# Performance work log

Hardware: AMD Instinct MI355X
Metric: run time of the kernel (lower is better)

Reference implementation:

```python
import jax, jax.numpy as jnp
import numpy as np

B, C, H = 16, 256, 32          # batch, in_channels(=out_channels), image_size
HEADS, HS = 8, 32              # heads = out_channels // head_size
D = HEADS * HS                 # head_dim = 256
N = H * H                      # tokens = 1024
EPS = 1e-5


def _rel_indices(h, w):
    # Faithful port of RelativeAttention2d.get_indices
    y = np.arange(h)
    x = np.arange(w)
    y1, x1, y2, x2 = np.meshgrid(y, x, y, x, indexing='ij')
    idx = (y1 - y2 + h - 1) * (2 * w - 1) + (x1 - x2 + w - 1)
    return jnp.asarray(idx.reshape(-1), dtype=jnp.int32)  # [N*N]


def setup_inputs() -> dict:
    key = jax.random.key(0)
    ks = jax.random.split(key, 10)
    s = 0.02
    return {
        'x': jax.random.normal(ks[0], (B, C, H, H), jnp.float32),
        'ln_g': jnp.ones((C,), jnp.float32),
        'ln_b': jnp.zeros((C,), jnp.float32),
        'wq': jax.random.normal(ks[1], (D, C), jnp.float32) * s,
        'bq': jnp.zeros((D,), jnp.float32),
        'wk': jax.random.normal(ks[2], (D, C), jnp.float32) * s,
        'bk': jnp.zeros((D,), jnp.float32),
        'wv': jax.random.normal(ks[3], (D, C), jnp.float32) * s,
        'bv': jnp.zeros((D,), jnp.float32),
        'wo': jax.random.normal(ks[4], (C, D), jnp.float32) * s,
        'bo': jnp.zeros((C,), jnp.float32),
        'rel_bias': jax.random.normal(ks[5], (HEADS, (2 * H - 1) * (2 * H - 1)), jnp.float32),
        'rel_idx': _rel_indices(H, H),
    }


def reference(x, ln_g, ln_b, wq, bq, wk, bk, wv, bv, wo, bo, rel_bias, rel_idx):
    b = x.shape[0]
    # norm(): LayerNorm over channel axis (dim 1 after the double transpose)
    mu = jnp.mean(x, axis=1, keepdims=True)
    var = jnp.mean((x - mu) ** 2, axis=1, keepdims=True)
    xn = (x - mu) / jnp.sqrt(var + EPS)
    xn = xn * ln_g[None, :, None, None] + ln_b[None, :, None, None]
    # reshape_for_linear: raw reshape [b, C, H, W] -> [b, N, C] (as in torch)
    xr = xn.reshape(b, N, C)
    # projections, then raw view(b, heads, head_size, -1) as in torch
    q = (xr @ wq.T + bq).reshape(b, HEADS, HS, N)
    k = (xr @ wk.T + bk).reshape(b, HEADS, HS, N)
    v = (xr @ wv.T + bv).reshape(b, HEADS, HS, N)
    # dots = k^T q / sqrt(head_dim)   [b, heads, N, N]
    dots = jnp.einsum('bhdn,bhdm->bhnm', k, q) / np.float32(np.sqrt(D))
    # gathered relative position bias  [heads, N, N]
    bias = rel_bias[:, rel_idx].reshape(HEADS, N, N)
    attn = jax.nn.softmax(dots + bias[None], axis=-2)  # non-standard softmax dim
    # out = v @ attn  [b, heads, head_size, N]
    out = jnp.einsum('bhdn,bhnm->bhdm', v, attn)
    out = out.reshape(b, H, H, D)  # raw view as in torch
    out = out @ wo.T + bo          # to_output linear (dropout is identity in eval)
    out = out.reshape(b, C, H, H)  # raw view back to [b, out_channels, H, W]
    return x + out
```

## Files before the change

kernel.cpp:

```cpp
#include <hip/hip_runtime.h>
#include <cstdint>

#define PERB 262144

typedef __attribute__((ext_vector_type(8))) short bf16x8;
typedef __attribute__((ext_vector_type(4))) float f32x4;
typedef unsigned short ushort_t;

__device__ __forceinline__ uint16_t f2bf(float f) {
    uint32_t u = __float_as_uint(f);
    u += 0x7fff + ((u >> 16) & 1);
    return (uint16_t)(u >> 16);
}

__global__ __launch_bounds__(256) void prep_kernel(
    const float* __restrict__ x, const float* __restrict__ gam,
    const float* __restrict__ bet, ushort_t* __restrict__ X,
    const float* __restrict__ wq, const float* __restrict__ wk,
    const float* __restrict__ wv, const float* __restrict__ wo,
    ushort_t* __restrict__ oq, ushort_t* __restrict__ ok,
    ushort_t* __restrict__ ov, ushort_t* __restrict__ oo)
{
    const int blk = blockIdx.x;
    const int tid = threadIdx.x;
    if (blk < 256) {
        const int which = blk >> 6;
        const int idx = ((blk & 63) * 256 + tid) * 4;
        const float* src = which == 0 ? wq : which == 1 ? wk : which == 2 ? wv : wo;
        ushort_t* dst    = which == 0 ? oq : which == 1 ? ok : which == 2 ? ov : oo;
        const float4 v = *(const float4*)&src[idx];
        uint2 p;
        p.x = (uint32_t)f2bf(v.x) | ((uint32_t)f2bf(v.y) << 16);
        p.y = (uint32_t)f2bf(v.z) | ((uint32_t)f2bf(v.w) << 16);
        *(uint2*)&dst[idx] = p;
        return;
    }
    const int lb  = blk - 256;
    const int b   = lb >> 5;
    const int sp0 = (lb & 31) << 5;
    const int spl = tid & 31;
    const int cg  = tid >> 5;
    const int c0  = cg << 5;
    const int sp  = sp0 + spl;
    const float* xb = x + (size_t)b * PERB + sp;

    float vals[32];
    float s = 0.f, sq = 0.f;
#pragma unroll
    for (int i = 0; i < 32; ++i) {
        float v = xb[(size_t)(c0 + i) * 1024];
        vals[i] = v; s += v; sq += v * v;
    }
    __shared__ float rs[8][32];
    __shared__ float rq[8][32];
    rs[cg][spl] = s; rq[cg][spl] = sq;
    __syncthreads();
    float ts = 0.f, tq = 0.f;
#pragma unroll
    for (int g = 0; g < 8; ++g) { ts += rs[g][spl]; tq += rq[g][spl]; }
    const float mean = ts * (1.f / 256.f);
    const float var  = tq * (1.f / 256.f) - mean * mean;
    const float rstd = rsqrtf(var + 1e-5f);

    ushort_t* Xb = X + (size_t)b * PERB + sp;
#pragma unroll
    for (int i = 0; i < 32; ++i) {
        const int cc = c0 + i;
        Xb[(size_t)cc * 1024] = f2bf((vals[i] - mean) * rstd * gam[cc] + bet[cc]);
    }
}

__global__ __launch_bounds__(256, 3) void qkv_kernel(
    const ushort_t* __restrict__ X,
    const ushort_t* __restrict__ wq, const float* __restrict__ bq,
    const ushort_t* __restrict__ wk, const float* __restrict__ bk,
    const ushort_t* __restrict__ wv, const float* __restrict__ bv,
    ushort_t* __restrict__ Q, ushort_t* __restrict__ K, ushort_t* __restrict__ V)
{
    __shared__ __align__(16) ushort_t Xl[512 * 8];
    __shared__ __align__(16) ushort_t Wl[3][512 * 8];

    const int blk = blockIdx.x;
    const int m0  = (blk >> 2) << 6;
    const int n0  = (blk & 3) << 6;
    const int tid = threadIdx.x;
    const int w    = tid >> 6;
    const int lane = tid & 63;
    const int quad = lane >> 4;
    const int c    = lane & 15;

    f32x4 acc[3][4];
#pragma unroll
    for (int o3 = 0; o3 < 3; ++o3)
#pragma unroll
        for (int i = 0; i < 4; ++i) acc[o3][i] = (f32x4){0.f, 0.f, 0.f, 0.f};

    for (int kc = 0; kc < 4; ++kc) {
        const int k0 = kc << 6;
        __syncthreads();
#pragma unroll
        for (int i = 0; i < 2; ++i) {
            const int id = tid + i * 256;
            const int kq = id >> 6, m = id & 63;
            *(bf16x8*)&Xl[id * 8] = *(const bf16x8*)&X[(size_t)(m0 + m) * 256 + k0 + kq * 8];
        }
#pragma unroll
        for (int i = 0; i < 2; ++i) {
            const int id = tid + i * 256;
            const int kq = id >> 6, n = id & 63;
            const size_t g = (size_t)(n0 + n) * 256 + k0 + kq * 8;
            *(bf16x8*)&Wl[0][id * 8] = *(const bf16x8*)&wq[g];
            *(bf16x8*)&Wl[1][id * 8] = *(const bf16x8*)&wk[g];
            *(bf16x8*)&Wl[2][id * 8] = *(const bf16x8*)&wv[g];
        }
        __syncthreads();
#pragma unroll
        for (int ks = 0; ks < 2; ++ks) {
            const int kq = ks * 4 + quad;
            bf16x8 af[4];
#pragma unroll
            for (int msub = 0; msub < 4; ++msub)
                af[msub] = *(const bf16x8*)&Xl[(kq * 64 + msub * 16 + c) * 8];
            bf16x8 bw[3];
#pragma unroll
            for (int o3 = 0; o3 < 3; ++o3)
                bw[o3] = *(const bf16x8*)&Wl[o3][(kq * 64 + w * 16 + c) * 8];
#pragma unroll
            for (int o3 = 0; o3 < 3; ++o3)
#pragma unroll
                for (int msub = 0; msub < 4; ++msub)
                    acc[o3][msub] = __builtin_amdgcn_mfma_f32_16x16x32_bf16(
                        bw[o3], af[msub], acc[o3][msub], 0, 0, 0);
        }
    }

    const int n = n0 + w * 16 + quad * 4;
    const float4 bq4 = *(const float4*)&bq[n];
    const float4 bk4 = *(const float4*)&bk[n];
    const float4 bv4 = *(const float4*)&bv[n];
    ushort_t* outs[3] = {Q, K, V};
    const float4 bias[3] = {bq4, bk4, bv4};
#pragma unroll
    for (int msub = 0; msub < 4; ++msub) {
        const size_t m = (size_t)(m0 + msub * 16 + c);
#pragma unroll
        for (int o3 = 0; o3 < 3; ++o3) {
            const f32x4 a = acc[o3][msub];
            uint2 p;
            p.x = (uint32_t)f2bf(a[0] + bias[o3].x) | ((uint32_t)f2bf(a[1] + bias[o3].y) << 16);
            p.y = (uint32_t)f2bf(a[2] + bias[o3].z) | ((uint32_t)f2bf(a[3] + bias[o3].w) << 16);
            *(uint2*)&outs[o3][m * 256 + n] = p;
        }
    }
}

#define C1F 0.09016844005556022f
#define LOG2EF 1.4426950408889634f

__global__ __launch_bounds__(256, 4) void attn_kernel(
    const ushort_t* __restrict__ Q, const ushort_t* __restrict__ K,
    const ushort_t* __restrict__ V, const float* __restrict__ relb,
    ushort_t* __restrict__ O)
{
    __shared__ __align__(16) unsigned char smem[20480];
    char* Pb = (char*)smem;
    char* Kl = (char*)(smem + 8192);
    char* Vl = (char*)(smem + 12288);

    const int blk = blockIdx.x;
    const int bh  = blk & 127;
    const int mt  = blk >> 7;
    const int b   = bh >> 3;
    const int h   = bh & 7;
    const int m0  = mt << 6;
    const int tid = threadIdx.x;
    const int w    = tid >> 6;
    const int lane = tid & 63;
    const int quad = lane >> 4;
    const int c    = lane & 15;

    const size_t base = (size_t)b * PERB + (size_t)h * 32768;
    const ushort_t* Qg = Q + base;
    const ushort_t* Kg = K + base;
    const ushort_t* Vg = V + base;
    const float* rbh = relb + h * 3969;

    {
        const int mm = tid & 63;
        const int sg = tid >> 6;
        union { bf16x8 v; uint16_t u[8]; } g0;
#pragma unroll
        for (int j = 0; j < 8; ++j)
            g0.u[j] = Qg[(size_t)(sg * 8 + j) * 1024 + m0 + mm];
        *(bf16x8*)(Pb + sg * 1024 + mm * 16) = g0.v;
    }
    __syncthreads();
    bf16x8 qfrag[4];
#pragma unroll
    for (int msub = 0; msub < 4; ++msub)
        qfrag[msub] = *(const bf16x8*)(Pb + quad * 1024 + (msub * 16 + c) * 16);

    int moff[4];
#pragma unroll
    for (int msub = 0; msub < 4; ++msub) {
        const int m = m0 + msub * 16 + c;
        moff[msub] = 1984 - (m >> 5) * 63 - (m & 31);
    }

    f32x4 oacc[2], dacc;
    dacc = (f32x4){0.f, 0.f, 0.f, 0.f};
#pragma unroll
    for (int j = 0; j < 2; ++j) oacc[j] = (f32x4){0.f, 0.f, 0.f, 0.f};
    bf16x8 onesf;
#pragma unroll
    for (int j = 0; j < 8; ++j) onesf[j] = (short)0x3F80;

    const int knn = tid & 63, ksg = tid >> 6;
    const int vs  = tid >> 3, vng = tid & 7;
    const int kWr = ksg * 1024 + knn * 16;
    const int vWr = vs * 128 + ((vng ^ (vs & 7)) << 4);
    const int kRd = quad * 1024 + (w * 16 + c) * 16;
    const int pWr = c * 128 + (((2 * w + (quad >> 1)) ^ (c & 7)) << 4) + ((quad & 1) << 3);
    const int c7  = c & 7;

    uint32_t kpre[8]; bf16x8 vpre;
#pragma unroll
    for (int j = 0; j < 8; ++j) kpre[j] = Kg[(size_t)(ksg * 8 + j) * 1024 + knn];
    vpre = *(const bf16x8*)&Vg[(size_t)vs * 1024 + vng * 8];

    for (int ch = 0; ch < 16; ++ch) {
        const int n0c = ch << 6;
        const int cb  = ch & 1;

        {
            uint4 kp;
            kp.x = kpre[0] | (kpre[1] << 16);
            kp.y = kpre[2] | (kpre[3] << 16);
            kp.z = kpre[4] | (kpre[5] << 16);
            kp.w = kpre[6] | (kpre[7] << 16);
            *(uint4*)(Kl + kWr) = kp;
            *(bf16x8*)(Vl + cb * 4096 + vWr) = vpre;
        }
        __syncthreads();

        {
            const int n0n = ((ch + 1) & 15) << 6;
#pragma unroll
            for (int j = 0; j < 8; ++j)
                kpre[j] = Kg[(size_t)(ksg * 8 + j) * 1024 + n0n + knn];
            vpre = *(const bf16x8*)&Vg[(size_t)vs * 1024 + n0n + vng * 8];
        }

        const bf16x8 kf = *(const bf16x8*)(Kl + kRd);
        f32x4 sacc[4];
#pragma unroll
        for (int msub = 0; msub < 4; ++msub) {
            const f32x4 z = {0.f, 0.f, 0.f, 0.f};
            sacc[msub] = __builtin_amdgcn_mfma_f32_16x16x32_bf16(kf, qfrag[msub], z, 0, 0, 0);
        }

        const int nbase = n0c + w * 16 + quad * 4;
        const int nidx0 = (nbase >> 5) * 63 + (nbase & 31);
#pragma unroll
        for (int msub = 0; msub < 4; ++msub) {
            const float* bp = rbh + nidx0 + moff[msub];
            float p[4];
#pragma unroll
            for (int r = 0; r < 4; ++r)
                p[r] = __builtin_amdgcn_exp2f(fmaf(bp[r], LOG2EF, sacc[msub][r] * C1F));
            uint2 pk;
            pk.x = __builtin_amdgcn_perm(__float_as_uint(p[1]), __float_as_uint(p[0]), 0x07060302u);
            pk.y = __builtin_amdgcn_perm(__float_as_uint(p[3]), __float_as_uint(p[2]), 0x07060302u);
            *(uint2*)(Pb + msub * 2048 + pWr) = pk;
        }
        __syncthreads();

#pragma unroll
        for (int kstep = 0; kstep < 2; ++kstep) {
            const int u = ((kstep * 4 + quad) ^ c7) << 4;
            const bf16x8 vf0 = *(const bf16x8*)(Vl + cb * 4096 + c * 128 + u);
            const bf16x8 vf1 = *(const bf16x8*)(Vl + cb * 4096 + (16 + c) * 128 + u);
            const bf16x8 pf  = *(const bf16x8*)(Pb + (w * 16 + c) * 128 + u);
            oacc[0] = __builtin_amdgcn_mfma_f32_16x16x32_bf16(vf0, pf, oacc[0], 0, 0, 0);
            oacc[1] = __builtin_amdgcn_mfma_f32_16x16x32_bf16(vf1, pf, oacc[1], 0, 0, 0);
            dacc    = __builtin_amdgcn_mfma_f32_16x16x32_bf16(onesf, pf, dacc, 0, 0, 0);
        }
    }

    ushort_t* Ob = O + base;
    const float inv = 1.0f / dacc[0];
    const int m = m0 + w * 16 + c;
#pragma unroll
    for (int ssub = 0; ssub < 2; ++ssub)
#pragma unroll
        for (int r = 0; r < 4; ++r)
            Ob[(size_t)(ssub * 16 + quad * 4 + r) * 1024 + m] = f2bf(oacc[ssub][r] * inv);
}

__global__ __launch_bounds__(256, 4) void oproj_kernel(
    const ushort_t* __restrict__ A, const ushort_t* __restrict__ wo,
    const float* __restrict__ bo, const float* __restrict__ x,
    float* __restrict__ out)
{
    __shared__ __align__(16) ushort_t Al[512 * 8];
    __shared__ __align__(16) ushort_t Wl[512 * 8];

    const int blk = blockIdx.x;
    const int m0  = (blk >> 2) << 6;
    const int n0  = (blk & 3) << 6;
    const int tid = threadIdx.x;
    const int w    = tid >> 6;
    const int lane = tid & 63;
    const int quad = lane >> 4;
    const int c    = lane & 15;

    f32x4 acc[4];
#pragma unroll
    for (int i = 0; i < 4; ++i) acc[i] = (f32x4){0.f, 0.f, 0.f, 0.f};

    for (int kc = 0; kc < 4; ++kc) {
        const int k0 = kc << 6;
        __syncthreads();
#pragma unroll
        for (int i = 0; i < 2; ++i) {
            const int id = tid + i * 256;
            const int kq = id >> 6, mn = id & 63;
            *(bf16x8*)&Al[id * 8] = *(const bf16x8*)&A [(size_t)(m0 + mn) * 256 + k0 + kq * 8];
            *(bf16x8*)&Wl[id * 8] = *(const bf16x8*)&wo[(size_t)(n0 + mn) * 256 + k0 + kq * 8];
        }
        __syncthreads();
#pragma unroll
        for (int ks = 0; ks < 2; ++ks) {
            const int kq = ks * 4 + quad;
            const bf16x8 bw = *(const bf16x8*)&Wl[(kq * 64 + w * 16 + c) * 8];
#pragma unroll
            for (int msub = 0; msub < 4; ++msub) {
                const bf16x8 af = *(const bf16x8*)&Al[(kq * 64 + msub * 16 + c) * 8];
                acc[msub] = __builtin_amdgcn_mfma_f32_16x16x32_bf16(bw, af, acc[msub], 0, 0, 0);
            }
        }
    }

    const int n = n0 + w * 16 + quad * 4;
    const float4 bo4 = *(const float4*)&bo[n];
#pragma unroll
    for (int msub = 0; msub < 4; ++msub) {
        const size_t g = (size_t)(m0 + msub * 16 + c) * 256 + n;
        const float4 r = *(const float4*)&x[g];
        float4 t;
        t.x = acc[msub][0] + bo4.x + r.x;
        t.y = acc[msub][1] + bo4.y + r.y;
        t.z = acc[msub][2] + bo4.z + r.z;
        t.w = acc[msub][3] + bo4.w + r.w;
        *(float4*)&out[g] = t;
    }
}

extern "C" void kernel_launch(void* const* d_in, const int* in_sizes, int n_in,
                              void* d_out, int out_size, void* d_ws, size_t ws_size,
                              hipStream_t stream)
{
    (void)in_sizes; (void)n_in; (void)out_size; (void)ws_size;
    const float* x   = (const float*)d_in[0];
    const float* lng = (const float*)d_in[1];
    const float* lnb = (const float*)d_in[2];
    const float* wq  = (const float*)d_in[3];
    const float* bq  = (const float*)d_in[4];
    const float* wk  = (const float*)d_in[5];
    const float* bk  = (const float*)d_in[6];
    const float* wv  = (const float*)d_in[7];
    const float* bv  = (const float*)d_in[8];
    const float* wo  = (const float*)d_in[9];
    const float* bo  = (const float*)d_in[10];
    const float* rb  = (const float*)d_in[11];

    ushort_t* ws = (ushort_t*)d_ws;
    ushort_t* Xbf = ws;
    ushort_t* Qbf = ws + 1 * 4194304;
    ushort_t* Kbf = ws + 2 * 4194304;
    ushort_t* Vbf = ws + 3 * 4194304;
    ushort_t* Obf = ws + 4 * 4194304;
    ushort_t* Wqb = ws + 5 * 4194304;
    ushort_t* Wkb = Wqb + 65536;
    ushort_t* Wvb = Wkb + 65536;
    ushort_t* Wob = Wvb + 65536;
    float* out = (float*)d_out;

    hipLaunchKernelGGL(prep_kernel,  dim3(768),  dim3(256), 0, stream,
                       x, lng, lnb, Xbf, wq, wk, wv, wo, Wqb, Wkb, Wvb, Wob);
    hipLaunchKernelGGL(qkv_kernel,   dim3(1024), dim3(256), 0, stream,
                       Xbf, Wqb, bq, Wkb, bk, Wvb, bv, Qbf, Kbf, Vbf);
    hipLaunchKernelGGL(attn_kernel,  dim3(2048), dim3(256), 0, stream, Qbf, Kbf, Vbf, rb, Obf);
    hipLaunchKernelGGL(oproj_kernel, dim3(1024), dim3(256), 0, stream, Obf, Wob, bo, x, out);
}
```

Measured before the change: 176.7 us.

## Store Q/K transposed from QKV kernel and double attention key chunk size

The QKV projection now writes Q and K in a per-head transposed layout, so the attention kernel can load them with 16-byte vector loads instead of scalar strided 2-byte gathers. The attention loop processes 128 keys per iteration instead of 64. This halves the number of barrier pairs and hoists relative-bias loads ahead of the score MFMAs. It also adds s_setprio around the MFMA sections. In exchange, the QKV epilogue does scattered scalar stores, and LDS per block doubles, with occupancy lowered to 3 blocks.

```diff
diff --git a/kernel.cpp b/kernel.cpp
--- a/kernel.cpp
+++ b/kernel.cpp
@@ -75,7 +75,7 @@
     const ushort_t* __restrict__ wq, const float* __restrict__ bq,
     const ushort_t* __restrict__ wk, const float* __restrict__ bk,
     const ushort_t* __restrict__ wv, const float* __restrict__ bv,
-    ushort_t* __restrict__ Q, ushort_t* __restrict__ K, ushort_t* __restrict__ V)
+    ushort_t* __restrict__ QT, ushort_t* __restrict__ KT, ushort_t* __restrict__ V)
 {
     __shared__ __align__(16) ushort_t Xl[512 * 8];
     __shared__ __align__(16) ushort_t Wl[3][512 * 8];
@@ -138,18 +138,24 @@
     const float4 bq4 = *(const float4*)&bq[n];
     const float4 bk4 = *(const float4*)&bk[n];
     const float4 bv4 = *(const float4*)&bv[n];
-    ushort_t* outs[3] = {Q, K, V};
-    const float4 bias[3] = {bq4, bk4, bv4};
+    const float bqa[4] = {bq4.x, bq4.y, bq4.z, bq4.w};
+    const float bka[4] = {bk4.x, bk4.y, bk4.z, bk4.w};
 #pragma unroll
     for (int msub = 0; msub < 4; ++msub) {
-        const size_t m = (size_t)(m0 + msub * 16 + c);
-#pragma unroll
-        for (int o3 = 0; o3 < 3; ++o3) {
-            const f32x4 a = acc[o3][msub];
-            uint2 p;
-            p.x = (uint32_t)f2bf(a[0] + bias[o3].x) | ((uint32_t)f2bf(a[1] + bias[o3].y) << 16);
-            p.y = (uint32_t)f2bf(a[2] + bias[o3].z) | ((uint32_t)f2bf(a[3] + bias[o3].w) << 16);
-            *(uint2*)&outs[o3][m * 256 + n] = p;
+        const int m = m0 + msub * 16 + c;
+        const f32x4 av = acc[2][msub];
+        uint2 pv;
+        pv.x = (uint32_t)f2bf(av[0] + bv4.x) | ((uint32_t)f2bf(av[1] + bv4.y) << 16);
+        pv.y = (uint32_t)f2bf(av[2] + bv4.z) | ((uint32_t)f2bf(av[3] + bv4.w) << 16);
+        *(uint2*)&V[(size_t)m * 256 + n] = pv;
+        const int tw = m & 1023;
+        const size_t tb = (size_t)(m >> 10) * 262144
+                        + (size_t)(tw >> 7) * 32768 + (size_t)((tw >> 2) & 31);
+        const int ta = (tw & 3) * 256 + n;
+#pragma unroll
+        for (int r = 0; r < 4; ++r) {
+            QT[tb + (size_t)(ta + r) * 32] = f2bf(acc[0][msub][r] + bqa[r]);
+            KT[tb + (size_t)(ta + r) * 32] = f2bf(acc[1][msub][r] + bka[r]);
         }
     }
 }
@@ -157,15 +163,15 @@
 #define C1F 0.09016844005556022f
 #define LOG2EF 1.4426950408889634f
 
-__global__ __launch_bounds__(256, 4) void attn_kernel(
-    const ushort_t* __restrict__ Q, const ushort_t* __restrict__ K,
+__global__ __launch_bounds__(256, 3) void attn_kernel(
+    const ushort_t* __restrict__ QT, const ushort_t* __restrict__ KT,
     const ushort_t* __restrict__ V, const float* __restrict__ relb,
     ushort_t* __restrict__ O)
 {
-    __shared__ __align__(16) unsigned char smem[20480];
+    __shared__ __align__(16) unsigned char smem[40960];
     char* Pb = (char*)smem;
-    char* Kl = (char*)(smem + 8192);
-    char* Vl = (char*)(smem + 12288);
+    char* Kl = (char*)(smem + 16384);
+    char* Vl = (char*)(smem + 24576);
 
     const int blk = blockIdx.x;
     const int bh  = blk & 127;
@@ -180,19 +186,16 @@
     const int c    = lane & 15;
 
     const size_t base = (size_t)b * PERB + (size_t)h * 32768;
-    const ushort_t* Qg = Q + base;
-    const ushort_t* Kg = K + base;
-    const ushort_t* Vg = V + base;
+    const ushort_t* QTg = QT + base;
+    const ushort_t* KTg = KT + base;
+    const ushort_t* Vg  = V + base;
     const float* rbh = relb + h * 3969;
 
     {
         const int mm = tid & 63;
         const int sg = tid >> 6;
-        union { bf16x8 v; uint16_t u[8]; } g0;
-#pragma unroll
-        for (int j = 0; j < 8; ++j)
-            g0.u[j] = Qg[(size_t)(sg * 8 + j) * 1024 + m0 + mm];
-        *(bf16x8*)(Pb + sg * 1024 + mm * 16) = g0.v;
+        const bf16x8 qv = *(const bf16x8*)&QTg[(size_t)(m0 + mm) * 32 + sg * 8];
+        *(bf16x8*)(Pb + sg * 1024 + mm * 16) = qv;
     }
     __syncthreads();
     bf16x8 qfrag[4];
@@ -217,74 +220,94 @@
 
     const int knn = tid & 63, ksg = tid >> 6;
     const int vs  = tid >> 3, vng = tid & 7;
-    const int kWr = ksg * 1024 + knn * 16;
-    const int vWr = vs * 128 + ((vng ^ (vs & 7)) << 4);
-    const int kRd = quad * 1024 + (w * 16 + c) * 16;
-    const int pWr = c * 128 + (((2 * w + (quad >> 1)) ^ (c & 7)) << 4) + ((quad & 1) << 3);
-    const int c7  = c & 7;
-
-    uint32_t kpre[8]; bf16x8 vpre;
-#pragma unroll
-    for (int j = 0; j < 8; ++j) kpre[j] = Kg[(size_t)(ksg * 8 + j) * 1024 + knn];
-    vpre = *(const bf16x8*)&Vg[(size_t)vs * 1024 + vng * 8];
-
-    for (int ch = 0; ch < 16; ++ch) {
-        const int n0c = ch << 6;
+    const int kWr  = ksg * 2048 + knn * 16;
+    const int vWr0 = vs * 256 + ((vng ^ (vs & 15)) << 4);
+    const int vWr1 = vs * 256 + (((vng + 8) ^ (vs & 15)) << 4);
+    const int kRd0 = quad * 2048 + (w * 32 + c) * 16;
+    const int kRd1 = quad * 2048 + (w * 32 + 16 + c) * 16;
+
+    bf16x8 kpre0, kpre1, vpre0, vpre1;
+    kpre0 = *(const bf16x8*)&KTg[(size_t)knn * 32 + ksg * 8];
+    kpre1 = *(const bf16x8*)&KTg[(size_t)(64 + knn) * 32 + ksg * 8];
+    vpre0 = *(const bf16x8*)&Vg[(size_t)vs * 1024 + vng * 8];
+    vpre1 = *(const bf16x8*)&Vg[(size_t)vs * 1024 + 64 + vng * 8];
+
+    for (int ch = 0; ch < 8; ++ch) {
+        const int n0c = ch << 7;
         const int cb  = ch & 1;
 
+        *(bf16x8*)(Kl + kWr)        = kpre0;
+        *(bf16x8*)(Kl + kWr + 1024) = kpre1;
+        *(bf16x8*)(Vl + cb * 8192 + vWr0) = vpre0;
+        *(bf16x8*)(Vl + cb * 8192 + vWr1) = vpre1;
+        __syncthreads();
+
+        float bb[4][2][4];
+#pragma unroll
+        for (int nsub = 0; nsub < 2; ++nsub) {
+            const int nbase = n0c + w * 32 + nsub * 16 + quad * 4;
+            const int nidx = (nbase >> 5) * 63 + (nbase & 31);
+#pragma unroll
+            for (int msub = 0; msub < 4; ++msub) {
+                const float* bp = rbh + nidx + moff[msub];
+#pragma unroll
+                for (int r = 0; r < 4; ++r) bb[msub][nsub][r] = bp[r];
+            }
+        }
+
         {
-            uint4 kp;
-            kp.x = kpre[0] | (kpre[1] << 16);
-            kp.y = kpre[2] | (kpre[3] << 16);
-            kp.z = kpre[4] | (kpre[5] << 16);
-            kp.w = kpre[6] | (kpre[7] << 16);
-            *(uint4*)(Kl + kWr) = kp;
-            *(bf16x8*)(Vl + cb * 4096 + vWr) = vpre;
-        }
-        __syncthreads();
-
-        {
-            const int n0n = ((ch + 1) & 15) << 6;
-#pragma unroll
-            for (int j = 0; j < 8; ++j)
-                kpre[j] = Kg[(size_t)(ksg * 8 + j) * 1024 + n0n + knn];
-            vpre = *(const bf16x8*)&Vg[(size_t)vs * 1024 + n0n + vng * 8];
-        }
-
-        const bf16x8 kf = *(const bf16x8*)(Kl + kRd);
-        f32x4 sacc[4];
+            const int n0n = ((ch + 1) & 7) << 7;
+            kpre0 = *(const bf16x8*)&KTg[(size_t)(n0n + knn) * 32 + ksg * 8];
+            kpre1 = *(const bf16x8*)&KTg[(size_t)(n0n + 64 + knn) * 32 + ksg * 8];
+            vpre0 = *(const bf16x8*)&Vg[(size_t)vs * 1024 + n0n + vng * 8];
+            vpre1 = *(const bf16x8*)&Vg[(size_t)vs * 1024 + n0n + 64 + vng * 8];
+        }
+
+        const bf16x8 kf0 = *(const bf16x8*)(Kl + kRd0);
+        const bf16x8 kf1 = *(const bf16x8*)(Kl + kRd1);
+        f32x4 sacc[4][2];
+        __builtin_amdgcn_s_setprio(1);
 #pragma unroll
         for (int msub = 0; msub < 4; ++msub) {
             const f32x4 z = {0.f, 0.f, 0.f, 0.f};
-            sacc[msub] = __builtin_amdgcn_mfma_f32_16x16x32_bf16(kf, qfrag[msub], z, 0, 0, 0);
-        }
-
-        const int nbase = n0c + w * 16 + quad * 4;
-        const int nidx0 = (nbase >> 5) * 63 + (nbase & 31);
+            sacc[msub][0] = __builtin_amdgcn_mfma_f32_16x16x32_bf16(kf0, qfrag[msub], z, 0, 0, 0);
+            sacc[msub][1] = __builtin_amdgcn_mfma_f32_16x16x32_bf16(kf1, qfrag[msub], z, 0, 0, 0);
+        }
+        __builtin_amdgcn_s_setprio(0);
+
 #pragma unroll
         for (int msub = 0; msub < 4; ++msub) {
-            const float* bp = rbh + nidx0 + moff[msub];
-            float p[4];
-#pragma unroll
-            for (int r = 0; r < 4; ++r)
-                p[r] = __builtin_amdgcn_exp2f(fmaf(bp[r], LOG2EF, sacc[msub][r] * C1F));
-            uint2 pk;
-            pk.x = __builtin_amdgcn_perm(__float_as_uint(p[1]), __float_as_uint(p[0]), 0x07060302u);
-            pk.y = __builtin_amdgcn_perm(__float_as_uint(p[3]), __float_as_uint(p[2]), 0x07060302u);
-            *(uint2*)(Pb + msub * 2048 + pWr) = pk;
-        }
-        __syncthreads();
-
-#pragma unroll
-        for (int kstep = 0; kstep < 2; ++kstep) {
-            const int u = ((kstep * 4 + quad) ^ c7) << 4;
-            const bf16x8 vf0 = *(const bf16x8*)(Vl + cb * 4096 + c * 128 + u);
-            const bf16x8 vf1 = *(const bf16x8*)(Vl + cb * 4096 + (16 + c) * 128 + u);
-            const bf16x8 pf  = *(const bf16x8*)(Pb + (w * 16 + c) * 128 + u);
+#pragma unroll
+            for (int nsub = 0; nsub < 2; ++nsub) {
+                float p[4];
+#pragma unroll
+                for (int r = 0; r < 4; ++r)
+                    p[r] = __builtin_amdgcn_exp2f(
+                        fmaf(bb[msub][nsub][r], LOG2EF, sacc[msub][nsub][r] * C1F));
+                uint2 pk;
+                pk.x = __builtin_amdgcn_perm(__float_as_uint(p[1]), __float_as_uint(p[0]), 0x07060302u);
+                pk.y = __builtin_amdgcn_perm(__float_as_uint(p[3]), __float_as_uint(p[2]), 0x07060302u);
+                const int pWr = (msub * 16 + c) * 256
+                              + (((4 * w + 2 * nsub + (quad >> 1)) ^ c) << 4)
+                              + ((quad & 1) << 3);
+                *(uint2*)(Pb + pWr) = pk;
+            }
+        }
+        __syncthreads();
+
+        const char* Vc = Vl + cb * 8192;
+        __builtin_amdgcn_s_setprio(1);
+#pragma unroll
+        for (int kstep = 0; kstep < 4; ++kstep) {
+            const int uu = ((kstep * 4 + quad) ^ c) << 4;
+            const bf16x8 vf0 = *(const bf16x8*)(Vc + c * 256 + uu);
+            const bf16x8 vf1 = *(const bf16x8*)(Vc + (16 + c) * 256 + uu);
+            const bf16x8 pf  = *(const bf16x8*)(Pb + (w * 16 + c) * 256 + uu);
             oacc[0] = __builtin_amdgcn_mfma_f32_16x16x32_bf16(vf0, pf, oacc[0], 0, 0, 0);
             oacc[1] = __builtin_amdgcn_mfma_f32_16x16x32_bf16(vf1, pf, oacc[1], 0, 0, 0);
             dacc    = __builtin_amdgcn_mfma_f32_16x16x32_bf16(onesf, pf, dacc, 0, 0, 0);
         }
+        __builtin_amdgcn_s_setprio(0);
     }
 
     ushort_t* Ob = O + base;
```

Measured after the change: 179.8 us. About the same (+1.8%).
